# Kernel tuning notes

Measured on AMD Instinct MI355X. Metric: run time of the kernel, lower is better.

The kernel has to match this reference:

```python
import jax, jax.numpy as jnp
import numpy as np

N_NODES = 100000
N_EDGES = 3200000
N_FEAT = 128
EMB = 64
HID = 64
N_SUB = 500000
N_GRAPHS = 1024
BN_EPS = 1e-5


def setup_inputs() -> dict:
    key = jax.random.key(0)
    ks = jax.random.split(key, 12)
    full_x = jax.random.normal(ks[0], (N_NODES, N_FEAT), dtype=jnp.float32)
    full_edge_index = jax.random.randint(ks[1], (2, N_EDGES), 0, N_NODES, dtype=jnp.int64)
    subgraph_node_indices = jax.random.randint(ks[2], (N_SUB,), 0, N_NODES, dtype=jnp.int64)
    batch_vector = jax.random.randint(ks[3], (N_SUB,), 0, N_GRAPHS, dtype=jnp.int64)
    # GCNConv params (glorot-style scale)
    W_enc = jax.random.normal(ks[4], (N_FEAT, EMB), dtype=jnp.float32) * (1.0 / np.sqrt(N_FEAT))
    b_enc = jnp.zeros((EMB,), dtype=jnp.float32)
    # predictor MLP params
    W1 = jax.random.normal(ks[5], (EMB, HID), dtype=jnp.float32) * (1.0 / np.sqrt(EMB))
    b1 = jnp.zeros((HID,), dtype=jnp.float32)
    gamma = jnp.ones((HID,), dtype=jnp.float32)
    beta = jnp.zeros((HID,), dtype=jnp.float32)
    W2 = jax.random.normal(ks[6], (HID, 1), dtype=jnp.float32) * (1.0 / np.sqrt(HID))
    b2 = jnp.zeros((1,), dtype=jnp.float32)
    return {
        "full_x": full_x,
        "full_edge_index": full_edge_index,
        "subgraph_node_indices": subgraph_node_indices,
        "batch_vector": batch_vector,
        "W_enc": W_enc, "b_enc": b_enc,
        "W1": W1, "b1": b1, "gamma": gamma, "beta": beta,
        "W2": W2, "b2": b2,
    }


def gcn_conv(x, edge_index, W, b):
    # PyG GCNConv: add self-loops, symmetric degree normalization, linear transform
    n = x.shape[0]
    loops = jnp.arange(n, dtype=edge_index.dtype)
    row = jnp.concatenate([edge_index[0], loops])  # source
    col = jnp.concatenate([edge_index[1], loops])  # target
    deg = jax.ops.segment_sum(jnp.ones_like(col, dtype=x.dtype), col, num_segments=n)
    dinv = jnp.where(deg > 0, jax.lax.rsqrt(deg), 0.0)
    norm = dinv[row] * dinv[col]  # [E+N]
    xw = x @ W  # transform first: [N, EMB]
    msgs = xw[row] * norm[:, None]
    out = jax.ops.segment_sum(msgs, col, num_segments=n)
    return out + b


def reference(full_x, full_edge_index, subgraph_node_indices, batch_vector,
              W_enc, b_enc, W1, b1, gamma, beta, W2, b2):
    # encoder + relu over all nodes
    h = jax.nn.relu(gcn_conv(full_x, full_edge_index, W_enc, b_enc))  # [N, EMB]
    # gather subgraph members
    sub = h[subgraph_node_indices]  # [N_SUB, EMB]
    # segment-mean pool into per-subgraph embeddings
    sums = jax.ops.segment_sum(sub, batch_vector, num_segments=N_GRAPHS)
    cnts = jax.ops.segment_sum(jnp.ones((sub.shape[0],), sub.dtype), batch_vector, num_segments=N_GRAPHS)
    pooled = sums / jnp.maximum(cnts, 1.0)[:, None]  # [N_GRAPHS, EMB]
    # predictor: Linear -> ReLU -> BatchNorm1d (training-mode batch stats) -> Linear
    z = jax.nn.relu(pooled @ W1 + b1)  # [N_GRAPHS, HID]
    mu = jnp.mean(z, axis=0)
    var = jnp.mean((z - mu) ** 2, axis=0)  # biased, as torch BN normalization
    zn = (z - mu) * jax.lax.rsqrt(var + BN_EPS) * gamma + beta
    return zn @ W2 + b2  # [N_GRAPHS, 1]
```

## Files before the change

kernel.cpp:

```cpp
#include <hip/hip_runtime.h>

#define N_NODES 100000
#define N_EDGES 3200000
#define N_FEAT 128
#define EMB 64
#define HID 64
#define N_SUB 500000
#define N_GRAPHS 1024
#define BN_EPS 1e-5f

#define NBKT 782
#define TILE 4096
#define NTILES 782
#define NGTILES 123
#define BKT_CAP 7168
#define GCAP 640
#define ZROW 100000
#define RPT 9

typedef __attribute__((ext_vector_type(8))) short short8;
typedef __attribute__((ext_vector_type(4))) float floatx4;

#define OFF_BCUR   0u
#define OFF_BCURG  4096u
#define OFF_BNSUM  8192u
#define ZERO_BYTES 8704u
#define OFF_DINV   12288u
#define OFF_OFFS   412672u
#define OFF_PAIRS  812672u
#define OFF_CSR    OFF_PAIRS
#define OFF_XWS    23235200u
#define OFF_SORTED 36035328u
#define OFF_H      38656768u
#define OFF_Z      51456896u

__device__ __forceinline__ bool is_bf(const unsigned* gamma_raw) {
  return (gamma_raw[0] & 0xFFFFu) != 0u;
}
__device__ __forceinline__ bool idx_is64(const int* subp) {
  return (subp[1] | subp[3] | subp[5] | subp[7]) == 0;
}
__device__ __forceinline__ float bf2f(ushort u) {
  union { unsigned i; float f; } v; v.i = ((unsigned)u) << 16; return v.f;
}
__device__ __forceinline__ ushort f2bf(float f) {
  union { float f; unsigned i; } v; v.f = f;
  unsigned lsb = (v.i >> 16) & 1u;
  v.i += 0x7FFFu + lsb;
  return (ushort)(v.i >> 16);
}
__device__ __forceinline__ float ld_f(const void* p, int i, bool bf) {
  return bf ? bf2f(((const ushort*)p)[i]) : ((const float*)p)[i];
}
__device__ __forceinline__ float lo_bf(unsigned d) {
  union { unsigned u; float f; } v; v.u = d << 16; return v.f;
}
__device__ __forceinline__ float hi_bf(unsigned d) {
  union { unsigned u; float f; } v; v.u = d & 0xFFFF0000u; return v.f;
}

__global__ __launch_bounds__(256) void k_scatsort(
    const int* e, const int* subp, const int* batch,
    int* bcur, unsigned* pairs, int* bcurg, int* sorted) {
  __shared__ int cnt[1024], lscan[1024], gbase[1024], wsum[4];
  __shared__ unsigned stage[TILE];
  __shared__ unsigned short stgb[TILE];
  bool w64 = idx_is64(subp);
  int tid = threadIdx.x, lane = tid & 63, wv = tid >> 6;
  bool edges = blockIdx.x < NTILES;
  int base = edges ? blockIdx.x * TILE : (blockIdx.x - NTILES) * TILE;
  int tot  = edges ? N_EDGES : N_SUB;
  int nb   = edges ? NBKT : N_GRAPHS;
  int tcnt = min(TILE, tot - base);
  int key[16], val[16];
  bool act = tid * 16 < tcnt;
  const int* kb = edges ? e : batch;
  const int* vb = edges ? e : subp;
  long long ko = edges ? (long long)N_EDGES : 0;
  if (act) {
    if (w64) {
      const int4* kp = (const int4*)kb + (ko + base) / 2 + tid * 8;
      const int4* vp = (const int4*)vb + base / 2 + tid * 8;
#pragma unroll
      for (int k = 0; k < 8; ++k) {
        int4 a = kp[k]; key[2 * k] = a.x; key[2 * k + 1] = a.z;
        int4 c = vp[k]; val[2 * k] = c.x; val[2 * k + 1] = c.z;
      }
    } else {
      const int4* kp = (const int4*)(kb + ko) + base / 4 + tid * 4;
      const int4* vp = (const int4*)vb + base / 4 + tid * 4;
#pragma unroll
      for (int k = 0; k < 4; ++k) {
        int4 a = kp[k];
        key[4 * k] = a.x; key[4 * k + 1] = a.y; key[4 * k + 2] = a.z; key[4 * k + 3] = a.w;
        int4 c = vp[k];
        val[4 * k] = c.x; val[4 * k + 1] = c.y; val[4 * k + 2] = c.z; val[4 * k + 3] = c.w;
      }
    }
  }
  for (int i = tid; i < 1024; i += 256) cnt[i] = 0;
  __syncthreads();
  if (act) {
#pragma unroll
    for (int k = 0; k < 16; ++k)
      atomicAdd(&cnt[edges ? (key[k] >> 7) : key[k]], 1);
  }
  __syncthreads();
  int b0 = tid * 4;
  int v0 = cnt[b0], v1 = cnt[b0 + 1], v2 = cnt[b0 + 2], v3 = cnt[b0 + 3];
  int s = v0 + v1 + v2 + v3, sc = s;
#pragma unroll
  for (int d = 1; d < 64; d <<= 1) {
    int t = __shfl_up(sc, d);
    if (lane >= d) sc += t;
  }
  if (lane == 63) wsum[wv] = sc;
  __syncthreads();
  int woff = 0;
#pragma unroll
  for (int w = 0; w < 4; ++w) woff += (w < wv) ? wsum[w] : 0;
  int excl = sc + woff - s;
  lscan[b0] = excl; lscan[b0 + 1] = excl + v0;
  lscan[b0 + 2] = excl + v0 + v1; lscan[b0 + 3] = excl + v0 + v1 + v2;
  __syncthreads();
  for (int b = tid; b < 1024; b += 256) {
    int c = (b < nb) ? cnt[b] : 0;
    gbase[b] = c ? (edges ? b * BKT_CAP + atomicAdd(&bcur[b], c)
                          : b * GCAP + atomicAdd(&bcurg[b], c)) : 0;
  }
  __syncthreads();
  for (int b = tid; b < 1024; b += 256) cnt[b] = 0;
  __syncthreads();
  if (act) {
#pragma unroll
    for (int k = 0; k < 16; ++k) {
      int b = edges ? (key[k] >> 7) : key[k];
      int r = atomicAdd(&cnt[b], 1);
      int p = lscan[b] + r;
      stage[p] = edges ? (((unsigned)(key[k] & 127) << 20) | (unsigned)val[k])
                       : (unsigned)val[k];
      stgb[p] = (unsigned short)b;
    }
  }
  __syncthreads();
  if (edges) {
    for (int j = tid; j < tcnt; j += 256) {
      int b = stgb[j];
      pairs[gbase[b] + (j - lscan[b])] = stage[j];
    }
  } else {
    for (int j = tid; j < tcnt; j += 256) {
      int b = stgb[j];
      sorted[gbase[b] + (j - lscan[b])] = (int)stage[j];
    }
  }
}

__global__ __launch_bounds__(512) void k_csr(
    const unsigned* __restrict__ pairs, const int* __restrict__ bcur,
    int* __restrict__ csr, unsigned* __restrict__ offs, float* __restrict__ dinv) {
  __shared__ int dl[128], loff[128], lcur[128];
  __shared__ int stage[BKT_CAP];
  __shared__ int ptot;
  int tid = threadIdx.x, b = blockIdx.x;
  if (tid < 128) dl[tid] = 0;
  __syncthreads();
  int s = b * BKT_CAP, cnt = bcur[b];
  unsigned pr[RPT];
#pragma unroll
  for (int k = 0; k < RPT; ++k) {
    int j = tid + k * 512;
    pr[k] = (j < cnt) ? pairs[s + j] : 0u;
  }
#pragma unroll
  for (int k = 0; k < RPT; ++k)
    if (tid + k * 512 < cnt) atomicAdd(&dl[pr[k] >> 20], 1);
  __syncthreads();
  int deg = 0, pd = 0;
  if (tid < 128) { deg = dl[tid]; pd = (deg + 31) & ~31; loff[tid] = pd; }
  __syncthreads();
  for (int d = 1; d < 128; d <<= 1) {
    int t = (tid >= d && tid < 128) ? loff[tid - d] : 0;
    __syncthreads();
    if (tid < 128) loff[tid] += t;
    __syncthreads();
  }
  if (tid < 128) {
    int excl = loff[tid] - pd;
    lcur[tid] = excl;
    int n = b * 128 + tid;
    if (n < N_NODES) {
      offs[n] = ((unsigned)(pd >> 5) << 24) | (unsigned)(s + excl);
      dinv[n] = rsqrtf((float)(deg + 1));
    }
    if (tid == 127) ptot = loff[127];
  }
  __syncthreads();
  int pt = ptot;
  for (int j = tid; j < pt; j += 512) stage[j] = ZROW;
  __syncthreads();
#pragma unroll
  for (int k = 0; k < RPT; ++k) {
    if (tid + k * 512 < cnt) {
      int pos = atomicAdd(&lcur[pr[k] >> 20], 1);
      stage[pos] = (int)(pr[k] & 0xFFFFF);
    }
  }
  __syncthreads();
  for (int j = tid; j < pt; j += 512) csr[s + j] = stage[j];
}

__global__ void k_gemm(const void* xraw, const void* Wraw, const unsigned* gamu,
                       const float* __restrict__ dinv, ushort* __restrict__ xws) {
  if (blockIdx.x == 0 && threadIdx.x < 32)
    ((unsigned*)xws)[(unsigned)ZROW * 32u + threadIdx.x] = 0u;
  bool bf = is_bf(gamu);
  const ushort* Wus = (const ushort*)Wraw;
  const float*  Wf  = (const float*)Wraw;
  int wv = threadIdx.x >> 6, lane = threadIdx.x & 63;
  int m = lane & 15, quad = lane >> 4;
  int c0 = wv * 16;
  short8 bfrag[4];
#pragma unroll
  for (int kc = 0; kc < 4; ++kc)
#pragma unroll
    for (int j = 0; j < 8; ++j) {
      int idx = (kc * 32 + quad * 8 + j) * EMB + c0 + m;
      bfrag[kc][j] = (short)(bf ? Wus[idx] : f2bf(Wf[idx]));
    }
  const ushort* xs = (const ushort*)xraw;
  const float*  xf = (const float*)xraw;
  for (int t = blockIdx.x; t < N_NODES / 16; t += gridDim.x) {
    int r0 = t * 16;
    floatx4 acc = {0.f, 0.f, 0.f, 0.f};
    if (bf) {
#pragma unroll
      for (int kc = 0; kc < 4; ++kc) {
        short8 a = *(const short8*)(xs + (r0 + m) * N_FEAT + kc * 32 + quad * 8);
        acc = __builtin_amdgcn_mfma_f32_16x16x32_bf16(a, bfrag[kc], acc, 0, 0, 0);
      }
    } else {
#pragma unroll
      for (int kc = 0; kc < 4; ++kc) {
        const float* ap = xf + (r0 + m) * N_FEAT + kc * 32 + quad * 8;
        float4 f0 = *(const float4*)ap, f1 = *(const float4*)(ap + 4);
        short8 a;
        a[0] = (short)f2bf(f0.x); a[1] = (short)f2bf(f0.y);
        a[2] = (short)f2bf(f0.z); a[3] = (short)f2bf(f0.w);
        a[4] = (short)f2bf(f1.x); a[5] = (short)f2bf(f1.y);
        a[6] = (short)f2bf(f1.z); a[7] = (short)f2bf(f1.w);
        acc = __builtin_amdgcn_mfma_f32_16x16x32_bf16(a, bfrag[kc], acc, 0, 0, 0);
      }
    }
#pragma unroll
    for (int r = 0; r < 4; ++r) {
      int row = r0 + quad * 4 + r;
      xws[row * EMB + c0 + m] = f2bf(acc[r] * dinv[row]);
    }
  }
}

#define ACCU(d) { aL0 += lo_bf(d.x); aH0 += hi_bf(d.x); aL1 += lo_bf(d.y); aH1 += hi_bf(d.y); \
                  aL2 += lo_bf(d.z); aH2 += hi_bf(d.z); aL3 += lo_bf(d.w); aH3 += hi_bf(d.w); }

__global__ void k_agg(const ushort* __restrict__ xws, const float* __restrict__ dinv,
                      const unsigned* __restrict__ offs, const int* __restrict__ csr,
                      const void* benc, const unsigned* gamu, ushort* __restrict__ h) {
  if (blockIdx.x == 0 && threadIdx.x < 32)
    ((unsigned*)h)[(unsigned)ZROW * 32u + threadIdx.x] = 0u;
  bool bf = is_bf(gamu);
  const uint4* xw4 = (const uint4*)xws;
  int wv = threadIdx.x >> 6, lane = threadIdx.x & 63;
  int e8 = lane >> 3, q = lane & 7;
  int n = blockIdx.x * 4 + wv;
  unsigned w = offs[n];
  int start = (int)(w & 0xFFFFFFu);
  int iters = (int)(w >> 24);
  float aL0 = 0.f, aH0 = 0.f, aL1 = 0.f, aH1 = 0.f, aL2 = 0.f, aH2 = 0.f, aL3 = 0.f, aH3 = 0.f;
  const int4* ip = (const int4*)(csr + start) + e8;
  for (int it = 0; it < iters; ++it) {
    int4 idx = ip[it * 8];
    uint4 u0 = xw4[idx.x * 8 + q];
    uint4 u1 = xw4[idx.y * 8 + q];
    uint4 u2 = xw4[idx.z * 8 + q];
    uint4 u3 = xw4[idx.w * 8 + q];
    ACCU(u0) ACCU(u1) ACCU(u2) ACCU(u3)
  }
#pragma unroll
  for (int msk = 8; msk < 64; msk <<= 1) {
    aL0 += __shfl_xor(aL0, msk); aH0 += __shfl_xor(aH0, msk);
    aL1 += __shfl_xor(aL1, msk); aH1 += __shfl_xor(aH1, msk);
    aL2 += __shfl_xor(aL2, msk); aH2 += __shfl_xor(aH2, msk);
    aL3 += __shfl_xor(aL3, msk); aH3 += __shfl_xor(aH3, msk);
  }
  if (e8 == 0) {
    float dn = dinv[n];
    uint4 us = xw4[n * 8 + q];
    ushort o[8];
    o[0] = f2bf(fmaxf((aL0 + lo_bf(us.x)) * dn + ld_f(benc, q * 8 + 0, bf), 0.f));
    o[1] = f2bf(fmaxf((aH0 + hi_bf(us.x)) * dn + ld_f(benc, q * 8 + 1, bf), 0.f));
    o[2] = f2bf(fmaxf((aL1 + lo_bf(us.y)) * dn + ld_f(benc, q * 8 + 2, bf), 0.f));
    o[3] = f2bf(fmaxf((aH1 + hi_bf(us.y)) * dn + ld_f(benc, q * 8 + 3, bf), 0.f));
    o[4] = f2bf(fmaxf((aL2 + lo_bf(us.z)) * dn + ld_f(benc, q * 8 + 4, bf), 0.f));
    o[5] = f2bf(fmaxf((aH2 + hi_bf(us.z)) * dn + ld_f(benc, q * 8 + 5, bf), 0.f));
    o[6] = f2bf(fmaxf((aL3 + lo_bf(us.w)) * dn + ld_f(benc, q * 8 + 6, bf), 0.f));
    o[7] = f2bf(fmaxf((aH3 + hi_bf(us.w)) * dn + ld_f(benc, q * 8 + 7, bf), 0.f));
    uint4 ov;
    ov.x = (unsigned)o[0] | ((unsigned)o[1] << 16);
    ov.y = (unsigned)o[2] | ((unsigned)o[3] << 16);
    ov.z = (unsigned)o[4] | ((unsigned)o[5] << 16);
    ov.w = (unsigned)o[6] | ((unsigned)o[7] << 16);
    ((uint4*)h)[n * 8 + q] = ov;
  }
}

__global__ void k_poolmlp1(const ushort* __restrict__ h, const int* __restrict__ sorted,
                           const int* __restrict__ bcurg, const void* W1, const void* b1,
                           const unsigned* gamu, float* __restrict__ z, float* bn) {
  bool bf = is_bf(gamu);
  __shared__ float red[4 * 64];
  __shared__ float pl[64];
  const uint4* h4 = (const uint4*)h;
  int g = blockIdx.x;
  int tid = threadIdx.x, wv = tid >> 6, lane = tid & 63;
  int e8 = lane >> 3, q = lane & 7;
  int start = g * GCAP, cnt = bcurg[g];
  int end = start + cnt;
  float aL0 = 0.f, aH0 = 0.f, aL1 = 0.f, aH1 = 0.f, aL2 = 0.f, aH2 = 0.f, aL3 = 0.f, aH3 = 0.f;
  for (int i = start + wv * 32; i < end; i += 128) {
#pragma unroll
    for (int c = 0; c < 4; ++c) {
      int idx = i + c * 8 + e8;
      int l = sorted[idx];
      int nn = (idx < end) ? l : ZROW;
      uint4 u = h4[nn * 8 + q];
      ACCU(u)
    }
  }
#pragma unroll
  for (int msk = 8; msk < 64; msk <<= 1) {
    aL0 += __shfl_xor(aL0, msk); aH0 += __shfl_xor(aH0, msk);
    aL1 += __shfl_xor(aL1, msk); aH1 += __shfl_xor(aH1, msk);
    aL2 += __shfl_xor(aL2, msk); aH2 += __shfl_xor(aH2, msk);
    aL3 += __shfl_xor(aL3, msk); aH3 += __shfl_xor(aH3, msk);
  }
  if (e8 == 0) {
    float* r = red + wv * 64 + q * 8;
    r[0] = aL0; r[1] = aH0; r[2] = aL1; r[3] = aH1;
    r[4] = aL2; r[5] = aH2; r[6] = aL3; r[7] = aH3;
  }
  __syncthreads();
  if (tid < 64) {
    float s = red[tid] + red[64 + tid] + red[128 + tid] + red[192 + tid];
    pl[tid] = s / fmaxf((float)cnt, 1.f);
  }
  __syncthreads();
  if (tid < 64) {
    int f = tid;
    float acc = ld_f(b1, f, bf);
#pragma unroll 8
    for (int k = 0; k < HID; ++k) acc += pl[k] * ld_f(W1, k * HID + f, bf);
    float zv = fmaxf(acc, 0.f);
    z[g * HID + f] = zv;
    atomicAdd(&bn[f], zv);
    atomicAdd(&bn[HID + f], zv * zv);
  }
}

__global__ void k_mlp2(const float* __restrict__ z, const float* __restrict__ bn,
                       const void* gmm, const void* beta, const void* W2, const void* b2,
                       const unsigned* gamu, void* out) {
  bool bf = is_bf(gamu);
  int wv = threadIdx.x >> 6, f = threadIdx.x & 63;
  int g = blockIdx.x * 4 + wv;
  float mu = bn[f] * (1.f / N_GRAPHS);
  float var = bn[HID + f] * (1.f / N_GRAPHS) - mu * mu;
  float zn = (z[g * HID + f] - mu) * rsqrtf(var + BN_EPS) * ld_f(gmm, f, bf) + ld_f(beta, f, bf);
  float val = zn * ld_f(W2, f, bf);
  for (int off = 32; off; off >>= 1) val += __shfl_down(val, off);
  if (f == 0) {
    val += ld_f(b2, 0, bf);
    if (bf) ((ushort*)out)[g] = f2bf(val);
    else    ((float*)out)[g]  = val;
  }
}

extern "C" void kernel_launch(void* const* d_in, const int* in_sizes, int n_in,
                              void* d_out, int out_size, void* d_ws, size_t ws_size,
                              hipStream_t stream) {
  const void* x_raw    = d_in[0];
  const int*  e_raw    = (const int*)d_in[1];
  const int*  sub_raw  = (const int*)d_in[2];
  const int*  bat_raw  = (const int*)d_in[3];
  const void* Wenc     = d_in[4];
  const void* benc     = d_in[5];
  const void* W1       = d_in[6];
  const void* b1       = d_in[7];
  const unsigned* gamu = (const unsigned*)d_in[8];
  const void* beta     = d_in[9];
  const void* W2       = d_in[10];
  const void* b2       = d_in[11];

  char* ws = (char*)d_ws;
  int*      bcur   = (int*)(ws + OFF_BCUR);
  int*      bcurg  = (int*)(ws + OFF_BCURG);
  float*    bnsum  = (float*)(ws + OFF_BNSUM);
  float*    dinv   = (float*)(ws + OFF_DINV);
  unsigned* offs   = (unsigned*)(ws + OFF_OFFS);
  unsigned* pairs  = (unsigned*)(ws + OFF_PAIRS);
  int*      csr    = (int*)(ws + OFF_CSR);
  ushort*   xws    = (ushort*)(ws + OFF_XWS);
  int*      sorted = (int*)(ws + OFF_SORTED);
  ushort*   h      = (ushort*)(ws + OFF_H);
  float*    z      = (float*)(ws + OFF_Z);

  hipMemsetAsync(ws, 0, ZERO_BYTES, stream);

  k_scatsort<<<NTILES + NGTILES, 256, 0, stream>>>(e_raw, sub_raw, bat_raw,
                                                   bcur, pairs, bcurg, sorted);
  k_csr     <<<NBKT, 512, 0, stream>>>(pairs, bcur, csr, offs, dinv);
  k_gemm    <<<1024, 256, 0, stream>>>(x_raw, Wenc, gamu, dinv, xws);
  k_agg     <<<N_NODES / 4, 256, 0, stream>>>(xws, dinv, offs, csr, benc, gamu, h);
  k_poolmlp1<<<N_GRAPHS, 256, 0, stream>>>(h, sorted, bcurg, W1, b1, gamu, z, bnsum);
  k_mlp2    <<<N_GRAPHS / 4, 256, 0, stream>>>(z, bnsum, gamu, beta, W2, b2, gamu, d_out);
}
```

Baseline: 281.1 us.

## Aggregate exact neighbor counts with chunked node loop instead of padded CSR slots

The CSR build now stores each node's true degree in the offset word and no longer fills the padded slots with a dummy zero-row index. The aggregation kernel handles the final partial group of 32 edges with predicated gathers, so it never loads the dummy row. It also switches to a fixed grid of 2048 blocks, each looping over 49 nodes, with the bias hoisted into registers and nontemporal loads for the index stream. This removes the padding fill pass and the wasted gathers, at the cost of divergent tail code and less parallel slack per block.

```diff
diff --git a/kernel.cpp b/kernel.cpp
--- a/kernel.cpp
+++ b/kernel.cpp
@@ -17,9 +17,12 @@
 #define GCAP 640
 #define ZROW 100000
 #define RPT 9
+#define NAGG_BLOCKS 2048
+#define NCHUNK 49
 
 typedef __attribute__((ext_vector_type(8))) short short8;
 typedef __attribute__((ext_vector_type(4))) float floatx4;
+typedef __attribute__((ext_vector_type(4))) int intx4;
 
 #define OFF_BCUR   0u
 #define OFF_BCURG  4096u
@@ -190,15 +193,13 @@
     lcur[tid] = excl;
     int n = b * 128 + tid;
     if (n < N_NODES) {
-      offs[n] = ((unsigned)(pd >> 5) << 24) | (unsigned)(s + excl);
+      offs[n] = ((unsigned)deg << 24) | (unsigned)(s + excl);
       dinv[n] = rsqrtf((float)(deg + 1));
     }
     if (tid == 127) ptot = loff[127];
   }
   __syncthreads();
   int pt = ptot;
-  for (int j = tid; j < pt; j += 512) stage[j] = ZROW;
-  __syncthreads();
 #pragma unroll
   for (int k = 0; k < RPT; ++k) {
     if (tid + k * 512 < cnt) {
@@ -263,54 +264,73 @@
 #define ACCU(d) { aL0 += lo_bf(d.x); aH0 += hi_bf(d.x); aL1 += lo_bf(d.y); aH1 += hi_bf(d.y); \
                   aL2 += lo_bf(d.z); aH2 += hi_bf(d.z); aL3 += lo_bf(d.w); aH3 += hi_bf(d.w); }
 
-__global__ void k_agg(const ushort* __restrict__ xws, const float* __restrict__ dinv,
-                      const unsigned* __restrict__ offs, const int* __restrict__ csr,
-                      const void* benc, const unsigned* gamu, ushort* __restrict__ h) {
+__global__ __launch_bounds__(256) void k_agg(
+    const ushort* __restrict__ xws, const float* __restrict__ dinv,
+    const unsigned* __restrict__ offs, const int* __restrict__ csr,
+    const void* benc, const unsigned* gamu, ushort* __restrict__ h) {
   if (blockIdx.x == 0 && threadIdx.x < 32)
     ((unsigned*)h)[(unsigned)ZROW * 32u + threadIdx.x] = 0u;
   bool bf = is_bf(gamu);
   const uint4* xw4 = (const uint4*)xws;
   int wv = threadIdx.x >> 6, lane = threadIdx.x & 63;
   int e8 = lane >> 3, q = lane & 7;
-  int n = blockIdx.x * 4 + wv;
-  unsigned w = offs[n];
-  int start = (int)(w & 0xFFFFFFu);
-  int iters = (int)(w >> 24);
-  float aL0 = 0.f, aH0 = 0.f, aL1 = 0.f, aH1 = 0.f, aL2 = 0.f, aH2 = 0.f, aL3 = 0.f, aH3 = 0.f;
-  const int4* ip = (const int4*)(csr + start) + e8;
-  for (int it = 0; it < iters; ++it) {
-    int4 idx = ip[it * 8];
-    uint4 u0 = xw4[idx.x * 8 + q];
-    uint4 u1 = xw4[idx.y * 8 + q];
-    uint4 u2 = xw4[idx.z * 8 + q];
-    uint4 u3 = xw4[idx.w * 8 + q];
-    ACCU(u0) ACCU(u1) ACCU(u2) ACCU(u3)
-  }
-#pragma unroll
-  for (int msk = 8; msk < 64; msk <<= 1) {
-    aL0 += __shfl_xor(aL0, msk); aH0 += __shfl_xor(aH0, msk);
-    aL1 += __shfl_xor(aL1, msk); aH1 += __shfl_xor(aH1, msk);
-    aL2 += __shfl_xor(aL2, msk); aH2 += __shfl_xor(aH2, msk);
-    aL3 += __shfl_xor(aL3, msk); aH3 += __shfl_xor(aH3, msk);
-  }
-  if (e8 == 0) {
-    float dn = dinv[n];
-    uint4 us = xw4[n * 8 + q];
-    ushort o[8];
-    o[0] = f2bf(fmaxf((aL0 + lo_bf(us.x)) * dn + ld_f(benc, q * 8 + 0, bf), 0.f));
-    o[1] = f2bf(fmaxf((aH0 + hi_bf(us.x)) * dn + ld_f(benc, q * 8 + 1, bf), 0.f));
-    o[2] = f2bf(fmaxf((aL1 + lo_bf(us.y)) * dn + ld_f(benc, q * 8 + 2, bf), 0.f));
-    o[3] = f2bf(fmaxf((aH1 + hi_bf(us.y)) * dn + ld_f(benc, q * 8 + 3, bf), 0.f));
-    o[4] = f2bf(fmaxf((aL2 + lo_bf(us.z)) * dn + ld_f(benc, q * 8 + 4, bf), 0.f));
-    o[5] = f2bf(fmaxf((aH2 + hi_bf(us.z)) * dn + ld_f(benc, q * 8 + 5, bf), 0.f));
-    o[6] = f2bf(fmaxf((aL3 + lo_bf(us.w)) * dn + ld_f(benc, q * 8 + 6, bf), 0.f));
-    o[7] = f2bf(fmaxf((aH3 + hi_bf(us.w)) * dn + ld_f(benc, q * 8 + 7, bf), 0.f));
-    uint4 ov;
-    ov.x = (unsigned)o[0] | ((unsigned)o[1] << 16);
-    ov.y = (unsigned)o[2] | ((unsigned)o[3] << 16);
-    ov.z = (unsigned)o[4] | ((unsigned)o[5] << 16);
-    ov.w = (unsigned)o[6] | ((unsigned)o[7] << 16);
-    ((uint4*)h)[n * 8 + q] = ov;
+  float bb[8];
+#pragma unroll
+  for (int j = 0; j < 8; ++j) bb[j] = ld_f(benc, q * 8 + j, bf);
+  int n0 = blockIdx.x * NCHUNK;
+  int nend = min(n0 + NCHUNK, N_NODES);
+  for (int n = n0 + wv; n < nend; n += 4) {
+    unsigned w = offs[n];
+    int start = (int)(w & 0xFFFFFFu);
+    int deg = (int)(w >> 24);
+    int full = deg >> 5, rem = deg & 31;
+    float aL0 = 0.f, aH0 = 0.f, aL1 = 0.f, aH1 = 0.f,
+          aL2 = 0.f, aH2 = 0.f, aL3 = 0.f, aH3 = 0.f;
+    const intx4* ip = (const intx4*)(csr + start) + e8;
+    for (int it = 0; it < full; ++it) {
+      intx4 idx = __builtin_nontemporal_load(ip + it * 8);
+      uint4 u0 = xw4[idx.x * 8 + q];
+      uint4 u1 = xw4[idx.y * 8 + q];
+      uint4 u2 = xw4[idx.z * 8 + q];
+      uint4 u3 = xw4[idx.w * 8 + q];
+      ACCU(u0) ACCU(u1) ACCU(u2) ACCU(u3)
+    }
+    if (rem) {
+      int sb = e8 * 4;
+      if (sb < rem) {
+        intx4 idx = __builtin_nontemporal_load(ip + full * 8);
+        { uint4 u = xw4[idx.x * 8 + q]; ACCU(u) }
+        if (sb + 1 < rem) { uint4 u = xw4[idx.y * 8 + q]; ACCU(u) }
+        if (sb + 2 < rem) { uint4 u = xw4[idx.z * 8 + q]; ACCU(u) }
+        if (sb + 3 < rem) { uint4 u = xw4[idx.w * 8 + q]; ACCU(u) }
+      }
+    }
+#pragma unroll
+    for (int msk = 8; msk < 64; msk <<= 1) {
+      aL0 += __shfl_xor(aL0, msk); aH0 += __shfl_xor(aH0, msk);
+      aL1 += __shfl_xor(aL1, msk); aH1 += __shfl_xor(aH1, msk);
+      aL2 += __shfl_xor(aL2, msk); aH2 += __shfl_xor(aH2, msk);
+      aL3 += __shfl_xor(aL3, msk); aH3 += __shfl_xor(aH3, msk);
+    }
+    if (e8 == 0) {
+      float dn = dinv[n];
+      uint4 us = xw4[n * 8 + q];
+      ushort o[8];
+      o[0] = f2bf(fmaxf((aL0 + lo_bf(us.x)) * dn + bb[0], 0.f));
+      o[1] = f2bf(fmaxf((aH0 + hi_bf(us.x)) * dn + bb[1], 0.f));
+      o[2] = f2bf(fmaxf((aL1 + lo_bf(us.y)) * dn + bb[2], 0.f));
+      o[3] = f2bf(fmaxf((aH1 + hi_bf(us.y)) * dn + bb[3], 0.f));
+      o[4] = f2bf(fmaxf((aL2 + lo_bf(us.z)) * dn + bb[4], 0.f));
+      o[5] = f2bf(fmaxf((aH2 + hi_bf(us.z)) * dn + bb[5], 0.f));
+      o[6] = f2bf(fmaxf((aL3 + lo_bf(us.w)) * dn + bb[6], 0.f));
+      o[7] = f2bf(fmaxf((aH3 + hi_bf(us.w)) * dn + bb[7], 0.f));
+      uint4 ov;
+      ov.x = (unsigned)o[0] | ((unsigned)o[1] << 16);
+      ov.y = (unsigned)o[2] | ((unsigned)o[3] << 16);
+      ov.z = (unsigned)o[4] | ((unsigned)o[5] << 16);
+      ov.w = (unsigned)o[6] | ((unsigned)o[7] << 16);
+      ((uint4*)h)[n * 8 + q] = ov;
+    }
   }
 }
 
@@ -420,7 +440,7 @@
                                                    bcur, pairs, bcurg, sorted);
   k_csr     <<<NBKT, 512, 0, stream>>>(pairs, bcur, csr, offs, dinv);
   k_gemm    <<<1024, 256, 0, stream>>>(x_raw, Wenc, gamu, dinv, xws);
-  k_agg     <<<N_NODES / 4, 256, 0, stream>>>(xws, dinv, offs, csr, benc, gamu, h);
+  k_agg     <<<NAGG_BLOCKS, 256, 0, stream>>>(xws, dinv, offs, csr, benc, gamu, h);
   k_poolmlp1<<<N_GRAPHS, 256, 0, stream>>>(h, sorted, bcurg, W1, b1, gamu, z, bnsum);
   k_mlp2    <<<N_GRAPHS / 4, 256, 0, stream>>>(z, bnsum, gamu, beta, W2, b2, gamu, d_out);
 }
```

Result: slower. 306.8 us (+9.1%).
